# Optimization experiments

Hardware: AMD Instinct MI355X
Metric: run time of the kernel (lower is better)

Reference implementation:

```python
import jax, jax.numpy as jnp
import numpy as np

N = 100000      # nodes
E = 1600000     # edges
G = 1000        # graphs in the batch
D_IN, D_H, D_OUT = 128, 128, 64


def setup_inputs() -> dict:
    key = jax.random.key(0)
    ks = jax.random.split(key, 8)
    x = jax.random.normal(ks[0], (N, D_IN), jnp.float32)
    edge_index = jax.random.randint(ks[1], (2, E), 0, N, dtype=jnp.int32)
    batch = jnp.sort(jax.random.randint(ks[2], (N,), 0, G, dtype=jnp.int32))
    s_in = 1.0 / np.sqrt(D_IN)
    s_h = 1.0 / np.sqrt(D_H)
    return {
        "x": x,
        "edge_index": edge_index,
        "batch": batch,
        "W_emb": jax.random.normal(ks[3], (D_IN, D_H), jnp.float32) * s_in,
        "b_emb": jnp.zeros((D_H,), jnp.float32),
        "W1": jax.random.normal(ks[4], (D_H, D_H), jnp.float32) * s_h,
        "b1": jnp.zeros((D_H,), jnp.float32),
        "W2": jax.random.normal(ks[5], (D_H, D_H), jnp.float32) * s_h,
        "b2": jnp.zeros((D_H,), jnp.float32),
        "W3": jax.random.normal(ks[6], (D_H, D_OUT), jnp.float32) * s_h,
        "b3": jnp.zeros((D_OUT,), jnp.float32),
    }


def reference(x, edge_index, batch, W_emb, b_emb, W1, b1, W2, b2, W3, b3):
    # Eval mode: dropout is identity.
    n = x.shape[0]
    src, dst = edge_index[0], edge_index[1]
    # GCN symmetric normalization with self-loops (Kipf & Welling).
    deg = jax.ops.segment_sum(jnp.ones(src.shape[0], x.dtype), dst, num_segments=n) + 1.0
    dis = jax.lax.rsqrt(deg)                 # deg^{-1/2}, [N]
    edge_norm = dis[src] * dis[dst]          # [E]
    self_norm = dis * dis                    # self-loop weight = 1/deg, [N]

    def gcn_conv(h, W, b):
        h = h @ W                                         # [N, d_out]
        agg = jax.ops.segment_sum(h[src] * edge_norm[:, None], dst, num_segments=n)
        return agg + h * self_norm[:, None] + b

    h = x @ W_emb + b_emb
    h = jax.nn.relu(gcn_conv(h, W1, b1))
    h = jax.nn.relu(gcn_conv(h, W2, b2))
    h = gcn_conv(h, W3, b3)
    # global_add_pool over graph ids
    return jax.ops.segment_sum(h, batch, num_segments=G)
```

## Files before the change

### kernel.cpp

```cpp
#include <hip/hip_runtime.h>
#include <hip/hip_bf16.h>

#define NN 100000
#define NE 1600000
#define NG 1000

typedef unsigned short u16;
typedef unsigned int u32;
typedef u16 u16x8 __attribute__((ext_vector_type(8)));
typedef u32 u32x4 __attribute__((ext_vector_type(4)));
typedef float f32x4 __attribute__((ext_vector_type(4)));
typedef __attribute__((ext_vector_type(8))) short s16x8;
typedef __attribute__((ext_vector_type(4))) float facc4;

__device__ __forceinline__ float bf2f(u16 u) {
    union { u32 i; float f; } c; c.i = ((u32)u) << 16; return c.f;
}
__device__ __forceinline__ u16 f2bf(float f) {
    __hip_bfloat16 h = __float2bfloat16(f);
    union { __hip_bfloat16 h; u16 u; } c; c.h = h; return c.u;
}

__global__ __launch_bounds__(256) void detect_kernel(const u32* __restrict__ xr, int* __restrict__ flag) {
    __shared__ int cnt[256];
    int c = 0;
    for (int i = threadIdx.x; i < 4096; i += 256) {
        u32 e = (xr[i] >> 7) & 0xFFu;
        if (e >= 110u && e <= 135u) c++;
    }
    cnt[threadIdx.x] = c;
    __syncthreads();
    for (int o = 128; o > 0; o >>= 1) {
        if (threadIdx.x < o) cnt[threadIdx.x] += cnt[threadIdx.x + o];
        __syncthreads();
    }
    if (threadIdx.x == 0) flag[0] = (cnt[0] > 2048) ? 1 : 0;
}

#define MEGA_NB 8039
__global__ __launch_bounds__(256) void mega_prep(
    const void* __restrict__ x, const int* __restrict__ flag, u16* __restrict__ xb,
    const void* __restrict__ Wemb, const void* __restrict__ W1, const void* __restrict__ W2,
    const void* __restrict__ W3, u16* __restrict__ wembT, u16* __restrict__ w1T,
    u16* __restrict__ w2T, u16* __restrict__ w3T,
    const void* __restrict__ bemb, const void* __restrict__ b1, const void* __restrict__ b2,
    const void* __restrict__ b3, float* __restrict__ bembF, float* __restrict__ b1F,
    float* __restrict__ b2F, float* __restrict__ b3F,
    const int* __restrict__ ei, int* __restrict__ counts)
{
    int b = blockIdx.x, tid = threadIdx.x;
    int fl = flag[0];
    if (b < 6250) {
        if (fl) return;
        int c = b * 256 + tid;
        f32x4 a = reinterpret_cast<const f32x4*>(x)[c * 2];
        f32x4 d = reinterpret_cast<const f32x4*>(x)[c * 2 + 1];
        u16x8 o;
        #pragma unroll
        for (int j = 0; j < 4; ++j) { o[j] = f2bf(a[j]); o[4 + j] = f2bf(d[j]); }
        reinterpret_cast<u16x8*>(xb)[c] = o;
    } else if (b < 6474) {
        int o = (b - 6250) * 256 + tid;
        const void* src; u16* dst; int M; int ol;
        if (o < 16384)      { src = Wemb; dst = wembT; M = 128; ol = o; }
        else if (o < 32768) { src = W1;   dst = w1T;   M = 128; ol = o - 16384; }
        else if (o < 49152) { src = W2;   dst = w2T;   M = 128; ol = o - 32768; }
        else                { src = W3;   dst = w3T;   M = 64;  ol = o - 49152; }
        int n = ol >> 7, k = ol & 127;
        u16 v = fl ? reinterpret_cast<const u16*>(src)[k * M + n]
                   : f2bf(reinterpret_cast<const float*>(src)[k * M + n]);
        dst[ol] = v;
    } else if (b < 6476) {
        int i = (b - 6474) * 256 + tid;
        if (i >= 448) return;
        const void* src; float* dst; int il;
        if (i < 128)      { src = bemb; dst = bembF; il = i; }
        else if (i < 256) { src = b1;   dst = b1F;   il = i - 128; }
        else if (i < 384) { src = b2;   dst = b2F;   il = i - 256; }
        else              { src = b3;   dst = b3F;   il = i - 384; }
        dst[il] = fl ? bf2f(reinterpret_cast<const u16*>(src)[il])
                     : reinterpret_cast<const float*>(src)[il];
    } else {
        int e0 = (b - 6476) * 1024 + tid * 4;
        if (e0 >= NE) return;
        int4 d4 = *reinterpret_cast<const int4*>(ei + NE + e0);
        atomicAdd(&counts[d4.x], 1);
        atomicAdd(&counts[d4.y], 1);
        atomicAdd(&counts[d4.z], 1);
        atomicAdd(&counts[d4.w], 1);
    }
}

__global__ __launch_bounds__(256) void scan1_kernel(const int* __restrict__ counts, int* __restrict__ offs,
                                                    int* __restrict__ bsums, float* __restrict__ dis,
                                                    int* __restrict__ cursor) {
    __shared__ int sums[256];
    int tid = threadIdx.x;
    int base = blockIdx.x * 2048 + tid * 8;
    int local[8];
    int s = 0;
    #pragma unroll
    for (int i = 0; i < 8; ++i) {
        int v = 0;
        if (base + i < NN) {
            v = counts[base + i];
            dis[base + i] = rsqrtf((float)v + 1.0f);
            cursor[base + i] = 0;
        }
        local[i] = s; s += v;
    }
    sums[tid] = s;
    __syncthreads();
    for (int o = 1; o < 256; o <<= 1) {
        int v = (tid >= o) ? sums[tid - o] : 0;
        __syncthreads();
        sums[tid] += v;
        __syncthreads();
    }
    int excl = sums[tid] - s;
    #pragma unroll
    for (int i = 0; i < 8; ++i)
        if (base + i < NN) offs[base + i] = excl + local[i];
    if (tid == 255) bsums[blockIdx.x] = sums[255];
}

__global__ __launch_bounds__(256) void scan3_kernel(int* __restrict__ offs, const int* __restrict__ bsums) {
    __shared__ int addv;
    int i = blockIdx.x * 256 + threadIdx.x;
    int bucket = blockIdx.x >> 3;
    if (threadIdx.x == 0) {
        int s = 0;
        for (int k = 0; k < bucket; ++k) s += bsums[k];
        addv = s;
    }
    __syncthreads();
    if (i < NN) offs[i] += addv;
}

__global__ __launch_bounds__(256) void scatter_kernel(const int* __restrict__ ei, const int* __restrict__ offs,
                                                      int* __restrict__ cursor, int* __restrict__ srcs) {
    int t = blockIdx.x * 256 + threadIdx.x;
    int e0 = t * 4;
    if (e0 >= NE) return;
    int4 s4 = *reinterpret_cast<const int4*>(ei + e0);
    int4 d4 = *reinterpret_cast<const int4*>(ei + NE + e0);
    int p0 = offs[d4.x] + atomicAdd(&cursor[d4.x], 1);
    int p1 = offs[d4.y] + atomicAdd(&cursor[d4.y], 1);
    int p2 = offs[d4.z] + atomicAdd(&cursor[d4.z], 1);
    int p3 = offs[d4.w] + atomicAdd(&cursor[d4.w], 1);
    srcs[p0] = s4.x;
    srcs[p1] = s4.y;
    srcs[p2] = s4.z;
    srcs[p3] = s4.w;
}

template <int M>
__global__ __launch_bounds__(256) void gemm_mfma(const u16* __restrict__ Hin, const u16* __restrict__ HinAlt,
                                                 const int* __restrict__ flag, const u16* __restrict__ Wt,
                                                 const float* __restrict__ bias, u16* __restrict__ Hout) {
    constexpr int LDW = 136;
    __shared__ u16 sW[M * LDW];
    int tid = threadIdx.x;
    const u16* A = (HinAlt != nullptr && flag[0]) ? HinAlt : Hin;
    for (int c = tid; c < M * 16; c += 256) {
        int n = c >> 4, kc = (c & 15) << 3;
        *reinterpret_cast<u16x8*>(sW + n * LDW + kc) = reinterpret_cast<const u16x8*>(Wt)[c];
    }
    __syncthreads();

    int wv = tid >> 6, lane = tid & 63;
    int m = lane & 15, quad = lane >> 4;
    int r0 = blockIdx.x * 64 + wv * 16;
    int ar = r0 + m; if (ar >= NN) ar = NN - 1;
    constexpr int NT = M / 16;
    facc4 acc[NT];
    #pragma unroll
    for (int t = 0; t < NT; ++t) acc[t] = (facc4){0.f, 0.f, 0.f, 0.f};

    const u16* arow = A + (size_t)ar * 128 + quad * 8;
    #pragma unroll
    for (int k0 = 0; k0 < 128; k0 += 32) {
        s16x8 a = *reinterpret_cast<const s16x8*>(arow + k0);
        #pragma unroll
        for (int t = 0; t < NT; ++t) {
            s16x8 bfr = *reinterpret_cast<const s16x8*>(sW + (t * 16 + m) * LDW + k0 + quad * 8);
            acc[t] = __builtin_amdgcn_mfma_f32_16x16x32_bf16(a, bfr, acc[t], 0, 0, 0);
        }
    }

    #pragma unroll
    for (int t = 0; t < NT; ++t) {
        int col = t * 16 + m;
        float bv = bias ? bias[col] : 0.0f;
        #pragma unroll
        for (int r = 0; r < 4; ++r) {
            int orow = r0 + quad * 4 + r;
            if (orow < NN)
                Hout[(size_t)orow * M + col] = f2bf(acc[t][r] + bv);
        }
    }
}

template <int MOUT>
__global__ __launch_bounds__(256) void fused_agg_gemm(const u16* __restrict__ T, const int* __restrict__ offs,
                                                      const int* __restrict__ counts, const float* __restrict__ dis,
                                                      const int* __restrict__ srcs, const float* __restrict__ aggbias,
                                                      const u16* __restrict__ Wt, u16* __restrict__ Hout) {
    constexpr int LDW = 136;
    __shared__ u16 sW[MOUT * LDW];
    __shared__ u16 sA[64 * LDW];
    int tid = threadIdx.x;
    for (int c = tid; c < MOUT * 16; c += 256) {
        int n = c >> 4, kc = (c & 15) << 3;
        *reinterpret_cast<u16x8*>(sW + n * LDW + kc) = reinterpret_cast<const u16x8*>(Wt)[c];
    }

    int lane = tid & 15, grp = tid >> 4;
    const u32x4* T4 = reinterpret_cast<const u32x4*>(T);
    for (int i = 0; i < 4; ++i) {
        int nl = grp * 4 + i;
        int n = blockIdx.x * 64 + nl;
        bool valid = n < NN;
        int nc = valid ? n : NN - 1;
        float di = dis[nc];
        float sn = di * di;
        u32x4 ts = T4[(size_t)nc * 16 + lane];
        float acc[8];
        #pragma unroll
        for (int q = 0; q < 4; ++q) {
            acc[2 * q]     = bf2f((u16)(ts[q] & 0xffffu)) * sn + aggbias[lane * 8 + 2 * q];
            acc[2 * q + 1] = bf2f((u16)(ts[q] >> 16))     * sn + aggbias[lane * 8 + 2 * q + 1];
        }
        int st = offs[nc], cnt = valid ? counts[nc] : 0;
        int j = 0;
        for (; j + 4 <= cnt; j += 4) {
            int e0 = srcs[st + j], e1 = srcs[st + j + 1], e2 = srcs[st + j + 2], e3 = srcs[st + j + 3];
            float w0 = dis[e0] * di, w1 = dis[e1] * di, w2 = dis[e2] * di, w3 = dis[e3] * di;
            u32x4 g0 = T4[(size_t)e0 * 16 + lane];
            u32x4 g1 = T4[(size_t)e1 * 16 + lane];
            u32x4 g2 = T4[(size_t)e2 * 16 + lane];
            u32x4 g3 = T4[(size_t)e3 * 16 + lane];
            #pragma unroll
            for (int q = 0; q < 4; ++q) {
                acc[2 * q]     += bf2f((u16)(g0[q] & 0xffffu)) * w0;
                acc[2 * q + 1] += bf2f((u16)(g0[q] >> 16))     * w0;
                acc[2 * q]     += bf2f((u16)(g1[q] & 0xffffu)) * w1;
                acc[2 * q + 1] += bf2f((u16)(g1[q] >> 16))     * w1;
                acc[2 * q]     += bf2f((u16)(g2[q] & 0xffffu)) * w2;
                acc[2 * q + 1] += bf2f((u16)(g2[q] >> 16))     * w2;
                acc[2 * q]     += bf2f((u16)(g3[q] & 0xffffu)) * w3;
                acc[2 * q + 1] += bf2f((u16)(g3[q] >> 16))     * w3;
            }
        }
        for (; j < cnt; ++j) {
            int e = srcs[st + j];
            float w = dis[e] * di;
            u32x4 g = T4[(size_t)e * 16 + lane];
            #pragma unroll
            for (int q = 0; q < 4; ++q) {
                acc[2 * q]     += bf2f((u16)(g[q] & 0xffffu)) * w;
                acc[2 * q + 1] += bf2f((u16)(g[q] >> 16))     * w;
            }
        }
        u16x8 pk;
        #pragma unroll
        for (int q = 0; q < 4; ++q) {
            pk[2 * q]     = f2bf(fmaxf(acc[2 * q], 0.0f));
            pk[2 * q + 1] = f2bf(fmaxf(acc[2 * q + 1], 0.0f));
        }
        *reinterpret_cast<u16x8*>(sA + nl * LDW + lane * 8) = pk;
    }
    __syncthreads();

    int wv = tid >> 6, l64 = tid & 63;
    int m = l64 & 15, quad = l64 >> 4;
    int r0 = blockIdx.x * 64 + wv * 16;
    constexpr int NT = MOUT / 16;
    facc4 gacc[NT];
    #pragma unroll
    for (int t = 0; t < NT; ++t) gacc[t] = (facc4){0.f, 0.f, 0.f, 0.f};
    #pragma unroll
    for (int k0 = 0; k0 < 128; k0 += 32) {
        s16x8 a = *reinterpret_cast<const s16x8*>(sA + (wv * 16 + m) * LDW + k0 + quad * 8);
        #pragma unroll
        for (int t = 0; t < NT; ++t) {
            s16x8 bfr = *reinterpret_cast<const s16x8*>(sW + (t * 16 + m) * LDW + k0 + quad * 8);
            gacc[t] = __builtin_amdgcn_mfma_f32_16x16x32_bf16(a, bfr, gacc[t], 0, 0, 0);
        }
    }
    #pragma unroll
    for (int t = 0; t < NT; ++t) {
        int col = t * 16 + m;
        #pragma unroll
        for (int r = 0; r < 4; ++r) {
            int orow = r0 + quad * 4 + r;
            if (orow < NN)
                Hout[(size_t)orow * MOUT + col] = f2bf(gacc[t][r]);
        }
    }
}

template <int M, bool RELU>
__global__ __launch_bounds__(256) void agg_kernel(const u16* __restrict__ T, const int* __restrict__ offs,
                                                  const int* __restrict__ counts, const float* __restrict__ dis,
                                                  const int* __restrict__ srcs, const float* __restrict__ bias,
                                                  u16* __restrict__ Hout) {
    constexpr int TPN = M / 8;
    constexpr int NPB = 256 / TPN;
    int lane = threadIdx.x % TPN;
    int n = blockIdx.x * NPB + threadIdx.x / TPN;
    if (n >= NN) return;
    const u32x4* T4 = reinterpret_cast<const u32x4*>(T);
    float di = dis[n];
    float sn = di * di;
    u32x4 ts = T4[(size_t)n * TPN + lane];
    float acc[8];
    #pragma unroll
    for (int q = 0; q < 4; ++q) {
        acc[2 * q]     = bf2f((u16)(ts[q] & 0xffffu)) * sn + bias[lane * 8 + 2 * q];
        acc[2 * q + 1] = bf2f((u16)(ts[q] >> 16))     * sn + bias[lane * 8 + 2 * q + 1];
    }
    int st = offs[n], cnt = counts[n];
    int j = 0;
    for (; j + 4 <= cnt; j += 4) {
        int e0 = srcs[st + j], e1 = srcs[st + j + 1], e2 = srcs[st + j + 2], e3 = srcs[st + j + 3];
        float w0 = dis[e0] * di, w1 = dis[e1] * di, w2 = dis[e2] * di, w3 = dis[e3] * di;
        u32x4 g0 = T4[(size_t)e0 * TPN + lane];
        u32x4 g1 = T4[(size_t)e1 * TPN + lane];
        u32x4 g2 = T4[(size_t)e2 * TPN + lane];
        u32x4 g3 = T4[(size_t)e3 * TPN + lane];
        #pragma unroll
        for (int q = 0; q < 4; ++q) {
            acc[2 * q]     += bf2f((u16)(g0[q] & 0xffffu)) * w0;
            acc[2 * q + 1] += bf2f((u16)(g0[q] >> 16))     * w0;
            acc[2 * q]     += bf2f((u16)(g1[q] & 0xffffu)) * w1;
            acc[2 * q + 1] += bf2f((u16)(g1[q] >> 16))     * w1;
            acc[2 * q]     += bf2f((u16)(g2[q] & 0xffffu)) * w2;
            acc[2 * q + 1] += bf2f((u16)(g2[q] >> 16))     * w2;
            acc[2 * q]     += bf2f((u16)(g3[q] & 0xffffu)) * w3;
            acc[2 * q + 1] += bf2f((u16)(g3[q] >> 16))     * w3;
        }
    }
    for (; j < cnt; ++j) {
        int e = srcs[st + j];
        float w = dis[e] * di;
        u32x4 g = T4[(size_t)e * TPN + lane];
        #pragma unroll
        for (int q = 0; q < 4; ++q) {
            acc[2 * q]     += bf2f((u16)(g[q] & 0xffffu)) * w;
            acc[2 * q + 1] += bf2f((u16)(g[q] >> 16))     * w;
        }
    }
    u32x4 ov;
    #pragma unroll
    for (int q = 0; q < 4; ++q) {
        float a0 = acc[2 * q], a1 = acc[2 * q + 1];
        if (RELU) { a0 = fmaxf(a0, 0.0f); a1 = fmaxf(a1, 0.0f); }
        ov[q] = (u32)f2bf(a0) | ((u32)f2bf(a1) << 16);
    }
    reinterpret_cast<u32x4*>(Hout)[(size_t)n * TPN + lane] = ov;
}

__global__ __launch_bounds__(64) void pool_kernel(const u16* __restrict__ H, const int* __restrict__ batch,
                                                  void* __restrict__ out, const int* __restrict__ flag) {
    int g = blockIdx.x;
    int f = threadIdx.x;
    int lo = 0, hi = NN;
    while (lo < hi) { int mid = (lo + hi) >> 1; if (batch[mid] < g) lo = mid + 1; else hi = mid; }
    int lo2 = lo, hi2 = NN;
    while (lo2 < hi2) { int mid = (lo2 + hi2) >> 1; if (batch[mid] < g + 1) lo2 = mid + 1; else hi2 = mid; }
    float acc = 0.0f;
    int n = lo;
    for (; n + 2 <= lo2; n += 2)
        acc += bf2f(H[(size_t)n * 64 + f]) + bf2f(H[(size_t)(n + 1) * 64 + f]);
    if (n < lo2) acc += bf2f(H[(size_t)n * 64 + f]);
    if (flag[0]) reinterpret_cast<u16*>(out)[g * 64 + f] = f2bf(acc);
    else         reinterpret_cast<float*>(out)[g * 64 + f] = acc;
}

extern "C" void kernel_launch(void* const* d_in, const int* in_sizes, int n_in,
                              void* d_out, int out_size, void* d_ws, size_t ws_size,
                              hipStream_t stream) {
    const void* x     = d_in[0];
    const int* ei     = (const int*)d_in[1];
    const int* batch  = (const int*)d_in[2];
    const void* W_emb = d_in[3];
    const void* b_emb = d_in[4];
    const void* W1    = d_in[5];
    const void* b1    = d_in[6];
    const void* W2    = d_in[7];
    const void* b2    = d_in[8];
    const void* W3    = d_in[9];
    const void* b3    = d_in[10];

    char* p = (char*)d_ws;
    auto alloc = [&](size_t bytes) { void* r = p; p += (bytes + 255) & ~(size_t)255; return r; };
    int*   flag   = (int*)alloc(256);
    int*   counts = (int*)alloc(NN * 4);
    int*   cursor = (int*)alloc(NN * 4);
    int*   offs   = (int*)alloc(NN * 4);
    float* dis    = (float*)alloc(NN * 4);
    int*   bsums  = (int*)alloc(256 * 4);
    int*   srcs   = (int*)alloc((size_t)NE * 4);
    u16*   wembT  = (u16*)alloc(128 * 128 * 2);
    u16*   w1T    = (u16*)alloc(128 * 128 * 2);
    u16*   w2T    = (u16*)alloc(128 * 128 * 2);
    u16*   w3T    = (u16*)alloc(64 * 128 * 2);
    float* bembF  = (float*)alloc(128 * 4);
    float* b1F    = (float*)alloc(128 * 4);
    float* b2F    = (float*)alloc(128 * 4);
    float* b3F    = (float*)alloc(64 * 4);
    u16*   hA     = (u16*)alloc((size_t)(NN + 64) * 128 * 2);
    u16*   hB     = (u16*)alloc((size_t)(NN + 64) * 128 * 2);

    hipMemsetAsync(counts, 0, NN * 4, stream);

    const int SB = (NN + 2047) / 2048;
    const int NB = (NN + 255) / 256;
    const int GB = (NN + 63) / 64;

    detect_kernel<<<1, 256, 0, stream>>>((const u32*)x, flag);
    mega_prep<<<MEGA_NB, 256, 0, stream>>>(x, flag, hB, W_emb, W1, W2, W3, wembT, w1T, w2T, w3T,
                                           b_emb, b1, b2, b3, bembF, b1F, b2F, b3F, ei, counts);
    scan1_kernel<<<SB, 256, 0, stream>>>(counts, offs, bsums, dis, cursor);
    scan3_kernel<<<NB, 256, 0, stream>>>(offs, bsums);
    scatter_kernel<<<(NE / 4 + 255) / 256, 256, 0, stream>>>(ei, offs, cursor, srcs);

    gemm_mfma<128><<<GB, 256, 0, stream>>>(hB, (const u16*)x, flag, wembT, bembF, hA);
    gemm_mfma<128><<<GB, 256, 0, stream>>>(hA, nullptr, flag, w1T, nullptr, hB);
    fused_agg_gemm<128><<<GB, 256, 0, stream>>>(hB, offs, counts, dis, srcs, b1F, w2T, hA);
    fused_agg_gemm<64><<<GB, 256, 0, stream>>>(hA, offs, counts, dis, srcs, b2F, w3T, hB);
    agg_kernel<64, false><<<(NN + 31) / 32, 256, 0, stream>>>(hB, offs, counts, dis, srcs, b3F, hA);
    pool_kernel<<<NG, 64, 0, stream>>>(hA, batch, d_out, flag);
}
```

Baseline: 543.2 us.

## Fuse edge scatter with embedding GEMM and final aggregation with graph pooling

Merges the CSR scatter pass into the embedding GEMM launch so the two independent jobs share one grid. The last aggregation is fused with global add pooling through shared-memory per-graph accumulators and float atomics, then a small kernel converts the result to the output dtype. Edge counting and scatter switch from four edges per thread to one, and reads of the source index list use nontemporal loads. This removes two launches and the intermediate H write and read for pooling, at the cost of atomics and nondeterministic summation order.

```diff
diff --git a/kernel.cpp b/kernel.cpp
--- a/kernel.cpp
+++ b/kernel.cpp
@@ -4,6 +4,7 @@
 #define NN 100000
 #define NE 1600000
 #define NG 1000
+#define SMAX 48
 
 typedef unsigned short u16;
 typedef unsigned int u32;
@@ -20,6 +21,7 @@
     __hip_bfloat16 h = __float2bfloat16(f);
     union { __hip_bfloat16 h; u16 u; } c; c.h = h; return c.u;
 }
+__device__ __forceinline__ int ntload(const int* p) { return __builtin_nontemporal_load(p); }
 
 __global__ __launch_bounds__(256) void detect_kernel(const u32* __restrict__ xr, int* __restrict__ flag) {
     __shared__ int cnt[256];
@@ -37,7 +39,7 @@
     if (threadIdx.x == 0) flag[0] = (cnt[0] > 2048) ? 1 : 0;
 }
 
-#define MEGA_NB 8039
+#define MEGA_NB 12726
 __global__ __launch_bounds__(256) void mega_prep(
     const void* __restrict__ x, const int* __restrict__ flag, u16* __restrict__ xb,
     const void* __restrict__ Wemb, const void* __restrict__ W1, const void* __restrict__ W2,
@@ -81,13 +83,8 @@
         dst[il] = fl ? bf2f(reinterpret_cast<const u16*>(src)[il])
                      : reinterpret_cast<const float*>(src)[il];
     } else {
-        int e0 = (b - 6476) * 1024 + tid * 4;
-        if (e0 >= NE) return;
-        int4 d4 = *reinterpret_cast<const int4*>(ei + NE + e0);
-        atomicAdd(&counts[d4.x], 1);
-        atomicAdd(&counts[d4.y], 1);
-        atomicAdd(&counts[d4.z], 1);
-        atomicAdd(&counts[d4.w], 1);
+        int e = (b - 6476) * 256 + tid;
+        if (e < NE) atomicAdd(&counts[ei[NE + e]], 1);
     }
 }
 
@@ -137,66 +134,93 @@
     if (i < NN) offs[i] += addv;
 }
 
-__global__ __launch_bounds__(256) void scatter_kernel(const int* __restrict__ ei, const int* __restrict__ offs,
-                                                      int* __restrict__ cursor, int* __restrict__ srcs) {
-    int t = blockIdx.x * 256 + threadIdx.x;
-    int e0 = t * 4;
-    if (e0 >= NE) return;
-    int4 s4 = *reinterpret_cast<const int4*>(ei + e0);
-    int4 d4 = *reinterpret_cast<const int4*>(ei + NE + e0);
-    int p0 = offs[d4.x] + atomicAdd(&cursor[d4.x], 1);
-    int p1 = offs[d4.y] + atomicAdd(&cursor[d4.y], 1);
-    int p2 = offs[d4.z] + atomicAdd(&cursor[d4.z], 1);
-    int p3 = offs[d4.w] + atomicAdd(&cursor[d4.w], 1);
-    srcs[p0] = s4.x;
-    srcs[p1] = s4.y;
-    srcs[p2] = s4.z;
-    srcs[p3] = s4.w;
-}
-
-template <int M>
-__global__ __launch_bounds__(256) void gemm_mfma(const u16* __restrict__ Hin, const u16* __restrict__ HinAlt,
-                                                 const int* __restrict__ flag, const u16* __restrict__ Wt,
-                                                 const float* __restrict__ bias, u16* __restrict__ Hout) {
-    constexpr int LDW = 136;
-    __shared__ u16 sW[M * LDW];
+__global__ __launch_bounds__(256) void mega2_kernel(
+    const u16* __restrict__ Hin, const u16* __restrict__ HinAlt, const int* __restrict__ flag,
+    const u16* __restrict__ Wt, const float* __restrict__ bias, u16* __restrict__ Hout,
+    const int* __restrict__ ei, const int* __restrict__ offs, int* __restrict__ cursor,
+    int* __restrict__ srcs)
+{
+    __shared__ u16 sW[128 * 136];
+    int b = blockIdx.x, tid = threadIdx.x;
+    if (b < 1563) {
+        const u16* A = flag[0] ? HinAlt : Hin;
+        for (int c = tid; c < 128 * 16; c += 256) {
+            int n = c >> 4, kc = (c & 15) << 3;
+            *reinterpret_cast<u16x8*>(sW + n * 136 + kc) = reinterpret_cast<const u16x8*>(Wt)[c];
+        }
+        __syncthreads();
+        int wv = tid >> 6, lane = tid & 63;
+        int m = lane & 15, quad = lane >> 4;
+        int r0 = b * 64 + wv * 16;
+        int ar = r0 + m; if (ar >= NN) ar = NN - 1;
+        facc4 acc[8];
+        #pragma unroll
+        for (int t = 0; t < 8; ++t) acc[t] = (facc4){0.f, 0.f, 0.f, 0.f};
+        const u16* arow = A + (size_t)ar * 128 + quad * 8;
+        #pragma unroll
+        for (int k0 = 0; k0 < 128; k0 += 32) {
+            s16x8 a = *reinterpret_cast<const s16x8*>(arow + k0);
+            #pragma unroll
+            for (int t = 0; t < 8; ++t) {
+                s16x8 bfr = *reinterpret_cast<const s16x8*>(sW + (t * 16 + m) * 136 + k0 + quad * 8);
+                acc[t] = __builtin_amdgcn_mfma_f32_16x16x32_bf16(a, bfr, acc[t], 0, 0, 0);
+            }
+        }
+        #pragma unroll
+        for (int t = 0; t < 8; ++t) {
+            int col = t * 16 + m;
+            float bv = bias[col];
+            #pragma unroll
+            for (int r = 0; r < 4; ++r) {
+                int orow = r0 + quad * 4 + r;
+                if (orow < NN)
+                    Hout[(size_t)orow * 128 + col] = f2bf(acc[t][r] + bv);
+            }
+        }
+    } else {
+        int e = (b - 1563) * 256 + tid;
+        if (e < NE) {
+            int s = ei[e], d = ei[NE + e];
+            int pos = offs[d] + atomicAdd(&cursor[d], 1);
+            srcs[pos] = s;
+        }
+    }
+}
+
+__global__ __launch_bounds__(256) void gemm_mfma128(const u16* __restrict__ Hin, const u16* __restrict__ Wt,
+                                                    u16* __restrict__ Hout) {
+    __shared__ u16 sW[128 * 136];
     int tid = threadIdx.x;
-    const u16* A = (HinAlt != nullptr && flag[0]) ? HinAlt : Hin;
-    for (int c = tid; c < M * 16; c += 256) {
+    for (int c = tid; c < 128 * 16; c += 256) {
         int n = c >> 4, kc = (c & 15) << 3;
-        *reinterpret_cast<u16x8*>(sW + n * LDW + kc) = reinterpret_cast<const u16x8*>(Wt)[c];
-    }
-    __syncthreads();
-
+        *reinterpret_cast<u16x8*>(sW + n * 136 + kc) = reinterpret_cast<const u16x8*>(Wt)[c];
+    }
+    __syncthreads();
     int wv = tid >> 6, lane = tid & 63;
     int m = lane & 15, quad = lane >> 4;
     int r0 = blockIdx.x * 64 + wv * 16;
     int ar = r0 + m; if (ar >= NN) ar = NN - 1;
-    constexpr int NT = M / 16;
-    facc4 acc[NT];
-    #pragma unroll
-    for (int t = 0; t < NT; ++t) acc[t] = (facc4){0.f, 0.f, 0.f, 0.f};
-
-    const u16* arow = A + (size_t)ar * 128 + quad * 8;
+    facc4 acc[8];
+    #pragma unroll
+    for (int t = 0; t < 8; ++t) acc[t] = (facc4){0.f, 0.f, 0.f, 0.f};
+    const u16* arow = Hin + (size_t)ar * 128 + quad * 8;
     #pragma unroll
     for (int k0 = 0; k0 < 128; k0 += 32) {
         s16x8 a = *reinterpret_cast<const s16x8*>(arow + k0);
         #pragma unroll
-        for (int t = 0; t < NT; ++t) {
-            s16x8 bfr = *reinterpret_cast<const s16x8*>(sW + (t * 16 + m) * LDW + k0 + quad * 8);
+        for (int t = 0; t < 8; ++t) {
+            s16x8 bfr = *reinterpret_cast<const s16x8*>(sW + (t * 16 + m) * 136 + k0 + quad * 8);
             acc[t] = __builtin_amdgcn_mfma_f32_16x16x32_bf16(a, bfr, acc[t], 0, 0, 0);
         }
     }
-
-    #pragma unroll
-    for (int t = 0; t < NT; ++t) {
+    #pragma unroll
+    for (int t = 0; t < 8; ++t) {
         int col = t * 16 + m;
-        float bv = bias ? bias[col] : 0.0f;
         #pragma unroll
         for (int r = 0; r < 4; ++r) {
             int orow = r0 + quad * 4 + r;
             if (orow < NN)
-                Hout[(size_t)orow * M + col] = f2bf(acc[t][r] + bv);
+                Hout[(size_t)orow * 128 + col] = f2bf(acc[t][r]);
         }
     }
 }
@@ -234,7 +258,10 @@
         int st = offs[nc], cnt = valid ? counts[nc] : 0;
         int j = 0;
         for (; j + 4 <= cnt; j += 4) {
-            int e0 = srcs[st + j], e1 = srcs[st + j + 1], e2 = srcs[st + j + 2], e3 = srcs[st + j + 3];
+            int e0 = ntload(srcs + st + j);
+            int e1 = ntload(srcs + st + j + 1);
+            int e2 = ntload(srcs + st + j + 2);
+            int e3 = ntload(srcs + st + j + 3);
             float w0 = dis[e0] * di, w1 = dis[e1] * di, w2 = dis[e2] * di, w3 = dis[e3] * di;
             u32x4 g0 = T4[(size_t)e0 * 16 + lane];
             u32x4 g1 = T4[(size_t)e1 * 16 + lane];
@@ -253,7 +280,7 @@
             }
         }
         for (; j < cnt; ++j) {
-            int e = srcs[st + j];
+            int e = ntload(srcs + st + j);
             float w = dis[e] * di;
             u32x4 g = T4[(size_t)e * 16 + lane];
             #pragma unroll
@@ -300,20 +327,24 @@
     }
 }
 
-template <int M, bool RELU>
-__global__ __launch_bounds__(256) void agg_kernel(const u16* __restrict__ T, const int* __restrict__ offs,
-                                                  const int* __restrict__ counts, const float* __restrict__ dis,
-                                                  const int* __restrict__ srcs, const float* __restrict__ bias,
-                                                  u16* __restrict__ Hout) {
-    constexpr int TPN = M / 8;
-    constexpr int NPB = 256 / TPN;
-    int lane = threadIdx.x % TPN;
-    int n = blockIdx.x * NPB + threadIdx.x / TPN;
-    if (n >= NN) return;
+__global__ __launch_bounds__(256) void agg_pool_kernel(const u16* __restrict__ T, const int* __restrict__ offs,
+                                                       const int* __restrict__ counts, const float* __restrict__ dis,
+                                                       const int* __restrict__ srcs, const float* __restrict__ bias,
+                                                       const int* __restrict__ batch, float* __restrict__ outF) {
+    __shared__ float accG[SMAX * 64];
+    __shared__ int sg0;
+    int tid = threadIdx.x;
+    for (int i = tid; i < SMAX * 64; i += 256) accG[i] = 0.0f;
+    if (tid == 0) sg0 = batch[blockIdx.x * 32];
+    __syncthreads();
+    int g0 = sg0;
+    int lane = tid & 7;
+    int n = blockIdx.x * 32 + (tid >> 3);
+
     const u32x4* T4 = reinterpret_cast<const u32x4*>(T);
     float di = dis[n];
     float sn = di * di;
-    u32x4 ts = T4[(size_t)n * TPN + lane];
+    u32x4 ts = T4[(size_t)n * 8 + lane];
     float acc[8];
     #pragma unroll
     for (int q = 0; q < 4; ++q) {
@@ -323,59 +354,64 @@
     int st = offs[n], cnt = counts[n];
     int j = 0;
     for (; j + 4 <= cnt; j += 4) {
-        int e0 = srcs[st + j], e1 = srcs[st + j + 1], e2 = srcs[st + j + 2], e3 = srcs[st + j + 3];
+        int e0 = ntload(srcs + st + j);
+        int e1 = ntload(srcs + st + j + 1);
+        int e2 = ntload(srcs + st + j + 2);
+        int e3 = ntload(srcs + st + j + 3);
         float w0 = dis[e0] * di, w1 = dis[e1] * di, w2 = dis[e2] * di, w3 = dis[e3] * di;
-        u32x4 g0 = T4[(size_t)e0 * TPN + lane];
-        u32x4 g1 = T4[(size_t)e1 * TPN + lane];
-        u32x4 g2 = T4[(size_t)e2 * TPN + lane];
-        u32x4 g3 = T4[(size_t)e3 * TPN + lane];
+        u32x4 g0v = T4[(size_t)e0 * 8 + lane];
+        u32x4 g1v = T4[(size_t)e1 * 8 + lane];
+        u32x4 g2v = T4[(size_t)e2 * 8 + lane];
+        u32x4 g3v = T4[(size_t)e3 * 8 + lane];
         #pragma unroll
         for (int q = 0; q < 4; ++q) {
-            acc[2 * q]     += bf2f((u16)(g0[q] & 0xffffu)) * w0;
-            acc[2 * q + 1] += bf2f((u16)(g0[q] >> 16))     * w0;
-            acc[2 * q]     += bf2f((u16)(g1[q] & 0xffffu)) * w1;
-            acc[2 * q + 1] += bf2f((u16)(g1[q] >> 16))     * w1;
-            acc[2 * q]     += bf2f((u16)(g2[q] & 0xffffu)) * w2;
-            acc[2 * q + 1] += bf2f((u16)(g2[q] >> 16))     * w2;
-            acc[2 * q]     += bf2f((u16)(g3[q] & 0xffffu)) * w3;
-            acc[2 * q + 1] += bf2f((u16)(g3[q] >> 16))     * w3;
+            acc[2 * q]     += bf2f((u16)(g0v[q] & 0xffffu)) * w0;
+            acc[2 * q + 1] += bf2f((u16)(g0v[q] >> 16))     * w0;
+            acc[2 * q]     += bf2f((u16)(g1v[q] & 0xffffu)) * w1;
+            acc[2 * q + 1] += bf2f((u16)(g1v[q] >> 16))     * w1;
+            acc[2 * q]     += bf2f((u16)(g2v[q] & 0xffffu)) * w2;
+            acc[2 * q + 1] += bf2f((u16)(g2v[q] >> 16))     * w2;
+            acc[2 * q]     += bf2f((u16)(g3v[q] & 0xffffu)) * w3;
+            acc[2 * q + 1] += bf2f((u16)(g3v[q] >> 16))     * w3;
         }
     }
     for (; j < cnt; ++j) {
-        int e = srcs[st + j];
+        int e = ntload(srcs + st + j);
         float w = dis[e] * di;
-        u32x4 g = T4[(size_t)e * TPN + lane];
+        u32x4 g = T4[(size_t)e * 8 + lane];
         #pragma unroll
         for (int q = 0; q < 4; ++q) {
             acc[2 * q]     += bf2f((u16)(g[q] & 0xffffu)) * w;
             acc[2 * q + 1] += bf2f((u16)(g[q] >> 16))     * w;
         }
     }
-    u32x4 ov;
-    #pragma unroll
-    for (int q = 0; q < 4; ++q) {
-        float a0 = acc[2 * q], a1 = acc[2 * q + 1];
-        if (RELU) { a0 = fmaxf(a0, 0.0f); a1 = fmaxf(a1, 0.0f); }
-        ov[q] = (u32)f2bf(a0) | ((u32)f2bf(a1) << 16);
-    }
-    reinterpret_cast<u32x4*>(Hout)[(size_t)n * TPN + lane] = ov;
-}
-
-__global__ __launch_bounds__(64) void pool_kernel(const u16* __restrict__ H, const int* __restrict__ batch,
-                                                  void* __restrict__ out, const int* __restrict__ flag) {
-    int g = blockIdx.x;
-    int f = threadIdx.x;
-    int lo = 0, hi = NN;
-    while (lo < hi) { int mid = (lo + hi) >> 1; if (batch[mid] < g) lo = mid + 1; else hi = mid; }
-    int lo2 = lo, hi2 = NN;
-    while (lo2 < hi2) { int mid = (lo2 + hi2) >> 1; if (batch[mid] < g + 1) lo2 = mid + 1; else hi2 = mid; }
-    float acc = 0.0f;
-    int n = lo;
-    for (; n + 2 <= lo2; n += 2)
-        acc += bf2f(H[(size_t)n * 64 + f]) + bf2f(H[(size_t)(n + 1) * 64 + f]);
-    if (n < lo2) acc += bf2f(H[(size_t)n * 64 + f]);
-    if (flag[0]) reinterpret_cast<u16*>(out)[g * 64 + f] = f2bf(acc);
-    else         reinterpret_cast<float*>(out)[g * 64 + f] = acc;
+
+    int s = batch[n] - g0;
+    if (s >= 0 && s < SMAX) {
+        #pragma unroll
+        for (int q = 0; q < 8; ++q)
+            atomicAdd(&accG[s * 64 + lane * 8 + q], acc[q]);
+    } else {
+        #pragma unroll
+        for (int q = 0; q < 8; ++q)
+            atomicAdd(&outF[(size_t)(g0 + s) * 64 + lane * 8 + q], acc[q]);
+    }
+    __syncthreads();
+    int gend = batch[blockIdx.x * 32 + 31];
+    int span = gend - g0 + 1;
+    if (span > SMAX) span = SMAX;
+    for (int i = tid; i < span * 64; i += 256)
+        atomicAdd(&outF[(size_t)g0 * 64 + i], accG[i]);
+}
+
+__global__ __launch_bounds__(256) void out_cvt_kernel(const float* __restrict__ outF, void* __restrict__ out,
+                                                      const int* __restrict__ flag) {
+    int i = blockIdx.x * 256 + threadIdx.x;
+    if (i < NG * 64) {
+        float v = outF[i];
+        if (flag[0]) reinterpret_cast<u16*>(out)[i] = f2bf(v);
+        else         reinterpret_cast<float*>(out)[i] = v;
+    }
 }
 
 extern "C" void kernel_launch(void* const* d_in, const int* in_sizes, int n_in,
@@ -410,10 +446,12 @@
     float* b1F    = (float*)alloc(128 * 4);
     float* b2F    = (float*)alloc(128 * 4);
     float* b3F    = (float*)alloc(64 * 4);
+    float* outF   = (float*)alloc((size_t)NG * 64 * 4);
     u16*   hA     = (u16*)alloc((size_t)(NN + 64) * 128 * 2);
     u16*   hB     = (u16*)alloc((size_t)(NN + 64) * 128 * 2);
 
     hipMemsetAsync(counts, 0, NN * 4, stream);
+    hipMemsetAsync(outF, 0, (size_t)NG * 64 * 4, stream);
 
     const int SB = (NN + 2047) / 2048;
     const int NB = (NN + 255) / 256;
@@ -424,12 +462,12 @@
                                            b_emb, b1, b2, b3, bembF, b1F, b2F, b3F, ei, counts);
     scan1_kernel<<<SB, 256, 0, stream>>>(counts, offs, bsums, dis, cursor);
     scan3_kernel<<<NB, 256, 0, stream>>>(offs, bsums);
-    scatter_kernel<<<(NE / 4 + 255) / 256, 256, 0, stream>>>(ei, offs, cursor, srcs);
-
-    gemm_mfma<128><<<GB, 256, 0, stream>>>(hB, (const u16*)x, flag, wembT, bembF, hA);
-    gemm_mfma<128><<<GB, 256, 0, stream>>>(hA, nullptr, flag, w1T, nullptr, hB);
+
+    mega2_kernel<<<GB + (NE + 255) / 256, 256, 0, stream>>>(hB, (const u16*)x, flag, wembT, bembF, hA,
+                                                            ei, offs, cursor, srcs);
+    gemm_mfma128<<<GB, 256, 0, stream>>>(hA, w1T, hB);
     fused_agg_gemm<128><<<GB, 256, 0, stream>>>(hB, offs, counts, dis, srcs, b1F, w2T, hA);
     fused_agg_gemm<64><<<GB, 256, 0, stream>>>(hA, offs, counts, dis, srcs, b2F, w3T, hB);
-    agg_kernel<64, false><<<(NN + 31) / 32, 256, 0, stream>>>(hB, offs, counts, dis, srcs, b3F, hA);
-    pool_kernel<<<NG, 64, 0, stream>>>(hA, batch, d_out, flag);
-}
+    agg_pool_kernel<<<NN / 32, 256, 0, stream>>>(hB, offs, counts, dis, srcs, b3F, batch, outF);
+    out_cvt_kernel<<<(NG * 64 + 255) / 256, 256, 0, stream>>>(outF, d_out, flag);
+}
```

New measurement: 577.2 us. 1.06x slower.
